# Kernel tuning notes

Measured on AMD Instinct MI355X. Metric: run time of the kernel, lower is better.

The kernel has to match this reference:

```python
import jax, jax.numpy as jnp
import numpy as np

NBITS = 4
DIM = 768
HEADS = 12
HEAD_DIM = DIM // HEADS
B, N = 8, 1024
SCALE = HEAD_DIM ** -0.5


def round_ste(x):
    # round_pass: straight-through round
    return x + jax.lax.stop_gradient(jnp.round(x) - x)


def grad_scale(x, g):
    # forward: x, backward: grad * g
    return x * g + jax.lax.stop_gradient(x * (1.0 - g))


def actq(x, alpha, zp, signed):
    # ActQ eval-mode forward: per-channel alpha/zero_point collapsed via .mean()
    if signed:
        Qn, Qp = -2 ** (NBITS - 1), 2 ** (NBITS - 1) - 1
    else:
        Qn, Qp = 0, 2 ** NBITS - 1
    a = jnp.mean(alpha)
    z = jnp.mean(round_ste(zp))
    xq = round_ste(jnp.clip(x / a + z, Qn, Qp))
    return (xq - z) * a


def linearq(x, w, b, alpha_w, act_alpha, act_zp):
    # LSQ weight quant (per-out-channel alpha with grad_scale) + input ActQ
    Qn, Qp = -2 ** (NBITS - 1), 2 ** (NBITS - 1) - 1
    g = 1.0 / np.sqrt(w.size * Qp)
    a = grad_scale(alpha_w, g)[:, None]  # [out,1]
    w_q = round_ste(jnp.clip(w / a, Qn, Qp)) * a
    xq = actq(x, act_alpha, act_zp, signed=True)
    y = jnp.einsum('...i,oi->...o', xq, w_q)
    return y if b is None else y + b


def layernorm(x, g, b, eps=1e-5):
    m = jnp.mean(x, axis=-1, keepdims=True)
    v = jnp.var(x, axis=-1, keepdims=True)  # biased, matches torch LayerNorm
    return (x - m) / jnp.sqrt(v + eps) * g + b


def setup_inputs() -> dict:
    key = jax.random.key(0)
    ks = jax.random.split(key, 20)
    u = lambda k, shape: jax.random.uniform(k, shape, jnp.float32, 0.01, 0.05)
    zp = lambda k, shape: jax.random.uniform(k, shape, jnp.float32, -0.3, 0.3)
    return {
        'x0': jax.random.normal(ks[0], (B, N, DIM), jnp.float32),
        'qkv_w': jax.random.normal(ks[1], (3 * DIM, DIM), jnp.float32) * 0.02,
        'qkv_alpha_w': u(ks[2], (3 * DIM,)),
        'qkv_act_alpha': u(ks[3], (DIM,)),
        'qkv_act_zp': zp(ks[4], (DIM,)),
        'norm_q_g': jnp.ones((HEAD_DIM,), jnp.float32),
        'norm_q_b': jnp.zeros((HEAD_DIM,), jnp.float32),
        'norm_k_g': jnp.ones((HEAD_DIM,), jnp.float32),
        'norm_k_b': jnp.zeros((HEAD_DIM,), jnp.float32),
        'q_alpha': u(ks[5], (HEADS,)), 'q_zp': zp(ks[6], (HEADS,)),
        'k_alpha': u(ks[7], (HEADS,)), 'k_zp': zp(ks[8], (HEADS,)),
        'v_alpha': u(ks[9], (HEADS,)), 'v_zp': zp(ks[10], (HEADS,)),
        'attn_alpha': u(ks[11], (HEADS,)), 'attn_zp': zp(ks[12], (HEADS,)),
        'proj_w': jax.random.normal(ks[13], (DIM, DIM), jnp.float32) * 0.02,
        'proj_b': jnp.zeros((DIM,), jnp.float32),
        'proj_alpha_w': u(ks[14], (DIM,)),
        'proj_act_alpha': u(ks[15], (DIM,)),
        'proj_act_zp': zp(ks[16], (DIM,)),
    }


def reference(x0, qkv_w, qkv_alpha_w, qkv_act_alpha, qkv_act_zp,
              norm_q_g, norm_q_b, norm_k_g, norm_k_b,
              q_alpha, q_zp, k_alpha, k_zp, v_alpha, v_zp,
              attn_alpha, attn_zp,
              proj_w, proj_b, proj_alpha_w, proj_act_alpha, proj_act_zp):
    b, n, c = x0.shape
    qkv = linearq(x0, qkv_w, None, qkv_alpha_w, qkv_act_alpha, qkv_act_zp)
    qkv = qkv.reshape(b, n, 3, HEADS, HEAD_DIM).transpose(2, 0, 3, 1, 4)  # [3,B,H,N,hd]
    q0, k0, v0 = qkv[0], qkv[1], qkv[2]
    q1 = layernorm(q0, norm_q_g, norm_q_b)
    k1 = layernorm(k0, norm_k_g, norm_k_b)
    q2 = actq(q1, q_alpha, q_zp, signed=True)
    k2 = actq(k1, k_alpha, k_zp, signed=True)
    v2 = actq(v0, v_alpha, v_zp, signed=True)
    attn = jax.nn.softmax(jnp.einsum('bhqd,bhkd->bhqk', q2, k2) * SCALE, axis=-1)
    attn = actq(attn, attn_alpha, attn_zp, signed=False)  # softmax output is unsigned
    x1 = jnp.einsum('bhqk,bhkd->bhqd', attn, v2).transpose(0, 2, 1, 3).reshape(b, n, c)
    return linearq(x1, proj_w, proj_b, proj_alpha_w, proj_act_alpha, proj_act_zp)
```

## Files before the change

kernel.cpp:

```cpp
#include <hip/hip_runtime.h>
#include <hip/hip_bf16.h>

#define HEADS 12
#define HD 64
#define DIM 768
#define SEQ 1024
#define NTOK 8192
#define TRIPLE 2304
#define BHTOT 96

typedef __attribute__((ext_vector_type(8))) short bf16x8;
typedef __attribute__((ext_vector_type(4))) float f32x4;

#define MFMA_B16(a, b, c) __builtin_amdgcn_mfma_f32_16x16x32_bf16((a), (b), (c), 0, 0, 0)

__device__ __forceinline__ unsigned short f2bf(float f) {
  unsigned int u = __float_as_uint(f);
  unsigned int r = (u + 0x7fffu + ((u >> 16) & 1u)) >> 16;
  return (unsigned short)r;
}
__device__ __forceinline__ float qclamp(float v, float lo, float hi) {
  return fminf(fmaxf(v, lo), hi);
}

__device__ float block_mean(const float* p, int n, int rnd, float* red) {
  int t = threadIdx.x;
  float s = 0.f;
  for (int i = t; i < n; i += 256) { float v = p[i]; s += rnd ? rintf(v) : v; }
  red[t] = s;
  __syncthreads();
  for (int o = 128; o > 0; o >>= 1) { if (t < o) red[t] += red[t + o]; __syncthreads(); }
  float m = red[0] / (float)n;
  __syncthreads();
  return m;
}

__global__ __launch_bounds__(256) void k_prep(
    const float* qaa, const float* qzp, const float* qa, const float* qz,
    const float* ka, const float* kz, const float* va, const float* vz,
    const float* ata, const float* atz, const float* pa, const float* pz,
    float* sc) {
  __shared__ float red[256];
  float r0 = block_mean(qaa, 768, 0, red);
  float r1 = block_mean(qzp, 768, 1, red);
  float r2 = block_mean(qa, 12, 0, red);
  float r3 = block_mean(qz, 12, 1, red);
  float r4 = block_mean(ka, 12, 0, red);
  float r5 = block_mean(kz, 12, 1, red);
  float r6 = block_mean(va, 12, 0, red);
  float r7 = block_mean(vz, 12, 1, red);
  float r8 = block_mean(ata, 12, 0, red);
  float r9 = block_mean(atz, 12, 1, red);
  float r10 = block_mean(pa, 768, 0, red);
  float r11 = block_mean(pz, 768, 1, red);
  if (threadIdx.x == 0) {
    sc[0] = r0; sc[1] = r1; sc[2] = r2; sc[3] = r3; sc[4] = r4; sc[5] = r5;
    sc[6] = r6; sc[7] = r7; sc[8] = r8; sc[9] = r9; sc[10] = r10; sc[11] = r11;
  }
}

__global__ __launch_bounds__(256) void k_quant_act(
    const float* __restrict__ x, unsigned short* __restrict__ xq,
    const float* __restrict__ sc, int n) {
  int i = (blockIdx.x * 256 + threadIdx.x) * 4;
  if (i >= n) return;
  float a = sc[0], z = sc[1];
  float4 v = *(const float4*)(x + i);
  ushort4 o;
  o.x = f2bf(rintf(qclamp(v.x / a + z, -8.f, 7.f)) - z);
  o.y = f2bf(rintf(qclamp(v.y / a + z, -8.f, 7.f)) - z);
  o.z = f2bf(rintf(qclamp(v.z / a + z, -8.f, 7.f)) - z);
  o.w = f2bf(rintf(qclamp(v.w / a + z, -8.f, 7.f)) - z);
  *(ushort4*)(xq + i) = o;
}

__global__ __launch_bounds__(256) void k_quant_w(
    const float* __restrict__ w, const float* __restrict__ alpha,
    unsigned short* __restrict__ wq, int n, int K) {
  int i = (blockIdx.x * 256 + threadIdx.x) * 4;
  if (i >= n) return;
  float a = alpha[i / K];
  float4 v = *(const float4*)(w + i);
  ushort4 o;
  o.x = f2bf(rintf(qclamp(v.x / a, -8.f, 7.f)));
  o.y = f2bf(rintf(qclamp(v.y / a, -8.f, 7.f)));
  o.z = f2bf(rintf(qclamp(v.z / a, -8.f, 7.f)));
  o.w = f2bf(rintf(qclamp(v.w / a, -8.f, 7.f)));
  *(ushort4*)(wq + i) = o;
}

__device__ __forceinline__ void stage128x64(
    const unsigned short* __restrict__ g, int ldk,
    unsigned short* lds, int wv, int l) {
#pragma unroll
  for (int j = 0; j < 4; ++j) {
    __builtin_amdgcn_global_load_lds(
        (const __attribute__((address_space(1))) void*)(
            g + (size_t)(wv * 32 + j * 8 + (l >> 3)) * ldk + (l & 7) * 8),
        (__attribute__((address_space(3))) void*)(lds + wv * 2048 + j * 512),
        16, 0, 0);
  }
}

__global__ __launch_bounds__(256) void k_gemm_qkv(
    const unsigned short* __restrict__ A, const unsigned short* __restrict__ Bw,
    const float* __restrict__ colscale, const float* __restrict__ sc,
    const float* __restrict__ nqg, const float* __restrict__ nqb,
    const float* __restrict__ nkg, const float* __restrict__ nkb,
    unsigned short* __restrict__ q2b, unsigned short* __restrict__ k2b,
    unsigned short* __restrict__ v2t) {
  __shared__ unsigned short As[128 * 64];
  __shared__ unsigned short Bs[128 * 64];
  const int t = threadIdx.x;
  const int brow = blockIdx.x * 128, bcol = blockIdx.y * 128;
  const int w = t >> 6, l = t & 63;
  const int lr = l & 15, lg = l >> 4;
  const int wr = (w >> 1) * 64, wc = (w & 1) * 64;
  f32x4 acc[4][4] = {};
  for (int kt = 0; kt < DIM; kt += 64) {
    __syncthreads();
    stage128x64(A + (size_t)brow * DIM + kt, DIM, As, w, l);
    stage128x64(Bw + (size_t)bcol * DIM + kt, DIM, Bs, w, l);
    __syncthreads();
#pragma unroll
    for (int ks = 0; ks < 2; ++ks) {
      bf16x8 af[4], bfr[4];
#pragma unroll
      for (int i = 0; i < 4; ++i) {
        af[i] = *(const bf16x8*)&As[(wr + i * 16 + lr) * 64 + ks * 32 + lg * 8];
        bfr[i] = *(const bf16x8*)&Bs[(wc + i * 16 + lr) * 64 + ks * 32 + lg * 8];
      }
#pragma unroll
      for (int i = 0; i < 4; ++i)
#pragma unroll
        for (int j = 0; j < 4; ++j)
          acc[i][j] = MFMA_B16(af[i], bfr[j], acc[i][j]);
    }
  }
  const float sact = sc[0];
  float s_j[4];
#pragma unroll
  for (int j = 0; j < 4; ++j) s_j[j] = sact * colscale[bcol + wc + j * 16 + lr];
#pragma unroll
  for (int i = 0; i < 4; ++i)
#pragma unroll
    for (int j = 0; j < 4; ++j)
#pragma unroll
      for (int r = 0; r < 4; ++r) acc[i][j][r] *= s_j[j];

  const int seg = bcol / DIM;
  const int h_ = ((bcol % DIM) + wc) / 64;
  if (seg < 2) {
    const float* gp = seg ? nkg : nqg;
    const float* bp = seg ? nkb : nqb;
    const float aq_ = seg ? sc[4] : sc[2];
    const float zq_ = seg ? sc[5] : sc[3];
    float gj[4], bj[4];
#pragma unroll
    for (int j = 0; j < 4; ++j) { gj[j] = gp[j * 16 + lr]; bj[j] = bp[j * 16 + lr]; }
    unsigned short* dstb = seg ? k2b : q2b;
#pragma unroll
    for (int i = 0; i < 4; ++i)
#pragma unroll
      for (int r = 0; r < 4; ++r) {
        float sum = acc[i][0][r] + acc[i][1][r] + acc[i][2][r] + acc[i][3][r];
        sum += __shfl_xor(sum, 1); sum += __shfl_xor(sum, 2);
        sum += __shfl_xor(sum, 4); sum += __shfl_xor(sum, 8);
        float m = sum * (1.0f / 64.0f);
        float vs = 0.f;
#pragma unroll
        for (int j = 0; j < 4; ++j) { float d = acc[i][j][r] - m; vs += d * d; }
        vs += __shfl_xor(vs, 1); vs += __shfl_xor(vs, 2);
        vs += __shfl_xor(vs, 4); vs += __shfl_xor(vs, 8);
        float inv = 1.0f / sqrtf(vs * (1.0f / 64.0f) + 1e-5f);
        int row = brow + wr + i * 16 + lg * 4 + r;
        int b_ = row >> 10, n_ = row & (SEQ - 1);
        unsigned short* dst = dstb + (((size_t)(b_ * HEADS + h_) << 10) + n_) * HD;
#pragma unroll
        for (int j = 0; j < 4; ++j) {
          float yv = (acc[i][j][r] - m) * inv * gj[j] + bj[j];
          float qv = rintf(qclamp(yv / aq_ + zq_, -8.f, 7.f)) - zq_;
          dst[j * 16 + lr] = f2bf(qv);
        }
      }
  } else {
    const float av_ = sc[6], zv = sc[7];
#pragma unroll
    for (int i = 0; i < 4; ++i)
#pragma unroll
      for (int r = 0; r < 4; ++r) {
        int row = brow + wr + i * 16 + lg * 4 + r;
        int b_ = row >> 10, n_ = row & (SEQ - 1);
        unsigned short* dst = v2t + ((size_t)(b_ * HEADS + h_) << 16) + n_;
#pragma unroll
        for (int j = 0; j < 4; ++j) {
          float qv = rintf(qclamp(acc[i][j][r] / av_ + zv, -8.f, 7.f)) - zv;
          dst[(size_t)(j * 16 + lr) * SEQ] = f2bf(qv);
        }
      }
  }
}

__global__ __launch_bounds__(256) void k_gemm(
    const unsigned short* __restrict__ A, const unsigned short* __restrict__ Bw,
    float* __restrict__ out, const float* __restrict__ colscale,
    const float* __restrict__ bias, const float* __restrict__ sc, int sact_idx,
    int M, int Nt, int K) {
  __shared__ unsigned short As[128 * 64];
  __shared__ unsigned short Bs[128 * 64];
  const int t = threadIdx.x;
  const int brow = blockIdx.x * 128, bcol = blockIdx.y * 128;
  const int w = t >> 6, l = t & 63;
  const int lr = l & 15, lg = l >> 4;
  const int wr = (w >> 1) * 64, wc = (w & 1) * 64;
  f32x4 acc[4][4] = {};
  for (int kt = 0; kt < K; kt += 64) {
    __syncthreads();
    stage128x64(A + (size_t)brow * K + kt, K, As, w, l);
    stage128x64(Bw + (size_t)bcol * K + kt, K, Bs, w, l);
    __syncthreads();
#pragma unroll
    for (int ks = 0; ks < 2; ++ks) {
      bf16x8 af[4], bfr[4];
#pragma unroll
      for (int i = 0; i < 4; ++i) {
        af[i] = *(const bf16x8*)&As[(wr + i * 16 + lr) * 64 + ks * 32 + lg * 8];
        bfr[i] = *(const bf16x8*)&Bs[(wc + i * 16 + lr) * 64 + ks * 32 + lg * 8];
      }
#pragma unroll
      for (int i = 0; i < 4; ++i)
#pragma unroll
        for (int j = 0; j < 4; ++j)
          acc[i][j] = MFMA_B16(af[i], bfr[j], acc[i][j]);
    }
  }
  const float sact = sc[sact_idx];
#pragma unroll
  for (int j = 0; j < 4; ++j) {
    const int col = bcol + wc + j * 16 + lr;
    const float s = sact * colscale[col];
    const float bb = bias ? bias[col] : 0.f;
#pragma unroll
    for (int i = 0; i < 4; ++i) {
      const int row0 = brow + wr + i * 16 + lg * 4;
#pragma unroll
      for (int r = 0; r < 4; ++r)
        out[(size_t)(row0 + r) * Nt + col] = acc[i][j][r] * s + bb;
    }
  }
}

__global__ __launch_bounds__(256, 3) void k_attn(
    const unsigned short* __restrict__ q2b, const unsigned short* __restrict__ k2b,
    const unsigned short* __restrict__ v2t, unsigned short* __restrict__ x1q,
    const float* __restrict__ sc) {
  __shared__ unsigned short Ks[128][72];
  __shared__ unsigned short Vs[64][136];
  __shared__ unsigned short Ps[4][32][40];
  const int t = threadIdx.x;
  const int w = t >> 6, l = t & 63;
  const int lr = l & 15, lg = l >> 4;
  const int bid = (int)(blockIdx.x & 7) * 96 + (int)(blockIdx.x >> 3);
  const int bh = bid >> 3, qc = bid & 7;
  const unsigned short* Qg = q2b + (size_t)bh * (SEQ * HD);
  const unsigned short* Kg = k2b + (size_t)bh * (SEQ * HD);
  const unsigned short* Vg = v2t + (size_t)bh * (SEQ * HD);
  const float aq = sc[2], ak = sc[4], av_ = sc[6], aa = sc[8], za = sc[9];
  const float ap = sc[10], zpp = sc[11];
  const float sqk2 = aq * ak * 0.125f * 1.44269504f;
  const float spv = aa * av_;
  const int qr0 = qc * 128 + w * 32;

  bf16x8 qf[2][2];
#pragma unroll
  for (int rt = 0; rt < 2; ++rt)
#pragma unroll
    for (int ks = 0; ks < 2; ++ks)
      qf[rt][ks] = *(const bf16x8*)(Qg + (size_t)(qr0 + rt * 16 + lr) * HD + ks * 32 + lg * 8);

  const int sr = t >> 1, sc0 = (t & 1) * 32;
  const int vr = t >> 2, vc0 = (t & 3) * 32;

  float lacc[2][4] = {};
  for (int kt = 0; kt < SEQ; kt += 128) {
    const uint4* g = (const uint4*)(Kg + (size_t)(kt + sr) * HD + sc0);
    uint4 u0 = g[0], u1 = g[1], u2 = g[2], u3 = g[3];
    __syncthreads();
    { uint4* d = (uint4*)&Ks[sr][sc0]; d[0] = u0; d[1] = u1; d[2] = u2; d[3] = u3; }
    __syncthreads();
#pragma unroll
    for (int ct = 0; ct < 8; ++ct) {
      const int kl = ct * 16 + lr;
      bf16x8 kf0 = *(const bf16x8*)&Ks[kl][lg * 8];
      bf16x8 kf1 = *(const bf16x8*)&Ks[kl][32 + lg * 8];
#pragma unroll
      for (int rt = 0; rt < 2; ++rt) {
        f32x4 s4 = {0.f, 0.f, 0.f, 0.f};
        s4 = MFMA_B16(qf[rt][0], kf0, s4);
        s4 = MFMA_B16(qf[rt][1], kf1, s4);
#pragma unroll
        for (int r = 0; r < 4; ++r)
          lacc[rt][r] += __builtin_amdgcn_exp2f(s4[r] * sqk2);
      }
    }
  }
#pragma unroll
  for (int off = 1; off < 16; off <<= 1)
#pragma unroll
    for (int rt = 0; rt < 2; ++rt)
#pragma unroll
      for (int r = 0; r < 4; ++r) lacc[rt][r] += __shfl_xor(lacc[rt][r], off);
  float pinv[2][4];
#pragma unroll
  for (int rt = 0; rt < 2; ++rt)
#pragma unroll
    for (int r = 0; r < 4; ++r) pinv[rt][r] = 1.0f / (lacc[rt][r] * aa);

  f32x4 oacc[2][4] = {};
  for (int kt = 0; kt < SEQ; kt += 128) {
    const uint4* gk = (const uint4*)(Kg + (size_t)(kt + sr) * HD + sc0);
    uint4 u0 = gk[0], u1 = gk[1], u2 = gk[2], u3 = gk[3];
    const uint4* gv = (const uint4*)(Vg + (size_t)vr * SEQ + kt + vc0);
    uint4 w0 = gv[0], w1 = gv[1], w2 = gv[2], w3 = gv[3];
    __syncthreads();
    { uint4* d = (uint4*)&Ks[sr][sc0]; d[0] = u0; d[1] = u1; d[2] = u2; d[3] = u3; }
    { uint4* d = (uint4*)&Vs[vr][vc0]; d[0] = w0; d[1] = w1; d[2] = w2; d[3] = w3; }
    __syncthreads();
#pragma unroll
    for (int q4 = 0; q4 < 4; ++q4) {
#pragma unroll
      for (int c2 = 0; c2 < 2; ++c2) {
        const int ct = q4 * 2 + c2;
        const int kl = ct * 16 + lr;
        bf16x8 kf0 = *(const bf16x8*)&Ks[kl][lg * 8];
        bf16x8 kf1 = *(const bf16x8*)&Ks[kl][32 + lg * 8];
#pragma unroll
        for (int rt = 0; rt < 2; ++rt) {
          f32x4 s4 = {0.f, 0.f, 0.f, 0.f};
          s4 = MFMA_B16(qf[rt][0], kf0, s4);
          s4 = MFMA_B16(qf[rt][1], kf1, s4);
#pragma unroll
          for (int r = 0; r < 4; ++r) {
            float e = __builtin_amdgcn_exp2f(s4[r] * sqk2);
            float p = fmaf(e, pinv[rt][r], za);
            float qv = rintf(qclamp(p, 0.f, 15.f)) - za;
            Ps[w][rt * 16 + lg * 4 + r][c2 * 16 + lr] = f2bf(qv);
          }
        }
      }
      bf16x8 vf[4], pf[2];
#pragma unroll
      for (int dt = 0; dt < 4; ++dt)
        vf[dt] = *(const bf16x8*)&Vs[dt * 16 + lr][q4 * 32 + lg * 8];
#pragma unroll
      for (int rt = 0; rt < 2; ++rt)
        pf[rt] = *(const bf16x8*)&Ps[w][rt * 16 + lr][lg * 8];
#pragma unroll
      for (int rt = 0; rt < 2; ++rt)
#pragma unroll
        for (int dt = 0; dt < 4; ++dt)
          oacc[rt][dt] = MFMA_B16(pf[rt], vf[dt], oacc[rt][dt]);
    }
  }
  const int b_ = bh / HEADS, h_ = bh % HEADS;
#pragma unroll
  for (int rt = 0; rt < 2; ++rt)
#pragma unroll
    for (int dt = 0; dt < 4; ++dt) {
      const int col = h_ * HD + dt * 16 + lr;
#pragma unroll
      for (int r = 0; r < 4; ++r) {
        const int qrow = qr0 + rt * 16 + lg * 4 + r;
        float x1v = oacc[rt][dt][r] * spv;
        float xv = rintf(qclamp(x1v / ap + zpp, -8.f, 7.f)) - zpp;
        x1q[(size_t)(b_ * SEQ + qrow) * DIM + col] = f2bf(xv);
      }
    }
}

extern "C" void kernel_launch(void* const* d_in, const int* in_sizes, int n_in,
                              void* d_out, int out_size, void* d_ws, size_t ws_size,
                              hipStream_t stream) {
  const float* x0      = (const float*)d_in[0];
  const float* qkvw    = (const float*)d_in[1];
  const float* qkv_aw  = (const float*)d_in[2];
  const float* qkv_aa  = (const float*)d_in[3];
  const float* qkv_azp = (const float*)d_in[4];
  const float* nqg     = (const float*)d_in[5];
  const float* nqb     = (const float*)d_in[6];
  const float* nkg     = (const float*)d_in[7];
  const float* nkb     = (const float*)d_in[8];
  const float* q_a     = (const float*)d_in[9];
  const float* q_z     = (const float*)d_in[10];
  const float* k_a     = (const float*)d_in[11];
  const float* k_z     = (const float*)d_in[12];
  const float* v_a     = (const float*)d_in[13];
  const float* v_z     = (const float*)d_in[14];
  const float* at_a    = (const float*)d_in[15];
  const float* at_z    = (const float*)d_in[16];
  const float* pw      = (const float*)d_in[17];
  const float* pb      = (const float*)d_in[18];
  const float* p_aw    = (const float*)d_in[19];
  const float* p_aa    = (const float*)d_in[20];
  const float* p_azp   = (const float*)d_in[21];
  float* out = (float*)d_out;

  char* ws = (char*)d_ws;
  size_t off = 0;
  float* scal = (float*)(ws); off = 256;
  unsigned short* x0q  = (unsigned short*)(ws + off); off += (size_t)NTOK * DIM * 2;
  unsigned short* qwq  = (unsigned short*)(ws + off); off += (size_t)TRIPLE * DIM * 2;
  unsigned short* pwq  = (unsigned short*)(ws + off); off += (size_t)DIM * DIM * 2;
  unsigned short* q2b  = (unsigned short*)(ws + off); off += (size_t)BHTOT * SEQ * HD * 2;
  unsigned short* k2b  = (unsigned short*)(ws + off); off += (size_t)BHTOT * SEQ * HD * 2;
  unsigned short* v2t  = (unsigned short*)(ws + off); off += (size_t)BHTOT * SEQ * HD * 2;
  unsigned short* x1q  = (unsigned short*)(ws + off); off += (size_t)NTOK * DIM * 2;

  k_prep<<<1, 256, 0, stream>>>(qkv_aa, qkv_azp, q_a, q_z, k_a, k_z, v_a, v_z,
                                at_a, at_z, p_aa, p_azp, scal);
  k_quant_act<<<(NTOK * DIM) / 1024, 256, 0, stream>>>(x0, x0q, scal, NTOK * DIM);
  k_quant_w<<<(TRIPLE * DIM) / 1024, 256, 0, stream>>>(qkvw, qkv_aw, qwq, TRIPLE * DIM, DIM);
  k_quant_w<<<(DIM * DIM) / 1024, 256, 0, stream>>>(pw, p_aw, pwq, DIM * DIM, DIM);
  k_gemm_qkv<<<dim3(NTOK / 128, TRIPLE / 128), 256, 0, stream>>>(
      x0q, qwq, qkv_aw, scal, nqg, nqb, nkg, nkb, q2b, k2b, v2t);
  k_attn<<<BHTOT * 8, 256, 0, stream>>>(q2b, k2b, v2t, x1q, scal);
  k_gemm<<<dim3(NTOK / 128, DIM / 128), 256, 0, stream>>>(
      x1q, pwq, out, p_aw, pb, scal, 10, NTOK, DIM, DIM);
}
```

Baseline: 291.1 us.

## Switch linear GEMMs to int8 MFMA with zero-point correction via weight row sums

Quantized activations and weights are now stored as int8 codes instead of bf16 values, and both linear GEMMs use the i32 16x16x64 int8 MFMA with K tiles of 128. Because the activation zero point is no longer folded into the stored values, a new kernel computes per-output-row weight sums so the epilogue can subtract zin*wsum before scaling. This halves the operand bytes and doubles the per-instruction K depth. The cost is an extra small kernel launch and exact integer-to-float conversions in the epilogue. The attention kernel now writes int8 codes for the projection input.

```diff
diff --git a/kernel.cpp b/kernel.cpp
--- a/kernel.cpp
+++ b/kernel.cpp
@@ -11,8 +11,10 @@
 
 typedef __attribute__((ext_vector_type(8))) short bf16x8;
 typedef __attribute__((ext_vector_type(4))) float f32x4;
+typedef __attribute__((ext_vector_type(4))) int i32x4;
 
 #define MFMA_B16(a, b, c) __builtin_amdgcn_mfma_f32_16x16x32_bf16((a), (b), (c), 0, 0, 0)
+#define MFMA_I8(a, b, c) __builtin_amdgcn_mfma_i32_16x16x64_i8((a), (b), (c), 0, 0, 0)
 
 __device__ __forceinline__ unsigned short f2bf(float f) {
   unsigned int u = __float_as_uint(f);
@@ -60,93 +62,114 @@
 }
 
 __global__ __launch_bounds__(256) void k_quant_act(
-    const float* __restrict__ x, unsigned short* __restrict__ xq,
+    const float* __restrict__ x, signed char* __restrict__ xq,
     const float* __restrict__ sc, int n) {
   int i = (blockIdx.x * 256 + threadIdx.x) * 4;
   if (i >= n) return;
   float a = sc[0], z = sc[1];
   float4 v = *(const float4*)(x + i);
-  ushort4 o;
-  o.x = f2bf(rintf(qclamp(v.x / a + z, -8.f, 7.f)) - z);
-  o.y = f2bf(rintf(qclamp(v.y / a + z, -8.f, 7.f)) - z);
-  o.z = f2bf(rintf(qclamp(v.z / a + z, -8.f, 7.f)) - z);
-  o.w = f2bf(rintf(qclamp(v.w / a + z, -8.f, 7.f)) - z);
-  *(ushort4*)(xq + i) = o;
+  int b0 = (int)rintf(qclamp(v.x / a + z, -8.f, 7.f));
+  int b1 = (int)rintf(qclamp(v.y / a + z, -8.f, 7.f));
+  int b2 = (int)rintf(qclamp(v.z / a + z, -8.f, 7.f));
+  int b3 = (int)rintf(qclamp(v.w / a + z, -8.f, 7.f));
+  ((int*)xq)[i >> 2] = (b0 & 255) | ((b1 & 255) << 8) | ((b2 & 255) << 16) | (b3 << 24);
 }
 
 __global__ __launch_bounds__(256) void k_quant_w(
     const float* __restrict__ w, const float* __restrict__ alpha,
-    unsigned short* __restrict__ wq, int n, int K) {
+    signed char* __restrict__ wq, int n, int K) {
   int i = (blockIdx.x * 256 + threadIdx.x) * 4;
   if (i >= n) return;
   float a = alpha[i / K];
   float4 v = *(const float4*)(w + i);
-  ushort4 o;
-  o.x = f2bf(rintf(qclamp(v.x / a, -8.f, 7.f)));
-  o.y = f2bf(rintf(qclamp(v.y / a, -8.f, 7.f)));
-  o.z = f2bf(rintf(qclamp(v.z / a, -8.f, 7.f)));
-  o.w = f2bf(rintf(qclamp(v.w / a, -8.f, 7.f)));
-  *(ushort4*)(wq + i) = o;
-}
-
-__device__ __forceinline__ void stage128x64(
-    const unsigned short* __restrict__ g, int ldk,
-    unsigned short* lds, int wv, int l) {
+  int b0 = (int)rintf(qclamp(v.x / a, -8.f, 7.f));
+  int b1 = (int)rintf(qclamp(v.y / a, -8.f, 7.f));
+  int b2 = (int)rintf(qclamp(v.z / a, -8.f, 7.f));
+  int b3 = (int)rintf(qclamp(v.w / a, -8.f, 7.f));
+  ((int*)wq)[i >> 2] = (b0 & 255) | ((b1 & 255) << 8) | ((b2 & 255) << 16) | (b3 << 24);
+}
+
+__global__ __launch_bounds__(256) void k_wsum(
+    const signed char* __restrict__ wq, float* __restrict__ s, int K) {
+  const int w = threadIdx.x >> 6, l = threadIdx.x & 63;
+  const int row = blockIdx.x * 4 + w;
+  const int* rp = (const int*)(wq + (size_t)row * K);
+  int acc = 0;
+  for (int idx = l; idx < K / 4; idx += 64) {
+    int u = rp[idx];
+    acc += (int)(signed char)u + (int)(signed char)(u >> 8) +
+           (int)(signed char)(u >> 16) + (int)(signed char)(u >> 24);
+  }
+#pragma unroll
+  for (int off = 32; off > 0; off >>= 1) acc += __shfl_xor(acc, off);
+  if (l == 0) s[row] = (float)acc;
+}
+
+__device__ __forceinline__ void stage_i8(
+    const signed char* __restrict__ g, int ldk,
+    signed char* lds, int wv, int l) {
 #pragma unroll
   for (int j = 0; j < 4; ++j) {
     __builtin_amdgcn_global_load_lds(
         (const __attribute__((address_space(1))) void*)(
-            g + (size_t)(wv * 32 + j * 8 + (l >> 3)) * ldk + (l & 7) * 8),
-        (__attribute__((address_space(3))) void*)(lds + wv * 2048 + j * 512),
+            g + (size_t)(wv * 32 + j * 8 + (l >> 3)) * ldk + (l & 7) * 16),
+        (__attribute__((address_space(3))) void*)(lds + wv * 4096 + j * 1024),
         16, 0, 0);
   }
 }
 
 __global__ __launch_bounds__(256) void k_gemm_qkv(
-    const unsigned short* __restrict__ A, const unsigned short* __restrict__ Bw,
-    const float* __restrict__ colscale, const float* __restrict__ sc,
+    const signed char* __restrict__ A, const signed char* __restrict__ Bw,
+    const float* __restrict__ colscale, const float* __restrict__ wsum,
+    const float* __restrict__ sc,
     const float* __restrict__ nqg, const float* __restrict__ nqb,
     const float* __restrict__ nkg, const float* __restrict__ nkb,
     unsigned short* __restrict__ q2b, unsigned short* __restrict__ k2b,
     unsigned short* __restrict__ v2t) {
-  __shared__ unsigned short As[128 * 64];
-  __shared__ unsigned short Bs[128 * 64];
+  __shared__ signed char As[128 * 128];
+  __shared__ signed char Bs[128 * 128];
   const int t = threadIdx.x;
   const int brow = blockIdx.x * 128, bcol = blockIdx.y * 128;
   const int w = t >> 6, l = t & 63;
   const int lr = l & 15, lg = l >> 4;
   const int wr = (w >> 1) * 64, wc = (w & 1) * 64;
-  f32x4 acc[4][4] = {};
-  for (int kt = 0; kt < DIM; kt += 64) {
-    __syncthreads();
-    stage128x64(A + (size_t)brow * DIM + kt, DIM, As, w, l);
-    stage128x64(Bw + (size_t)bcol * DIM + kt, DIM, Bs, w, l);
+  i32x4 acc[4][4] = {};
+  for (int kt = 0; kt < DIM; kt += 128) {
+    __syncthreads();
+    stage_i8(A + (size_t)brow * DIM + kt, DIM, As, w, l);
+    stage_i8(Bw + (size_t)bcol * DIM + kt, DIM, Bs, w, l);
     __syncthreads();
 #pragma unroll
     for (int ks = 0; ks < 2; ++ks) {
-      bf16x8 af[4], bfr[4];
+      i32x4 af[4], bfr[4];
 #pragma unroll
       for (int i = 0; i < 4; ++i) {
-        af[i] = *(const bf16x8*)&As[(wr + i * 16 + lr) * 64 + ks * 32 + lg * 8];
-        bfr[i] = *(const bf16x8*)&Bs[(wc + i * 16 + lr) * 64 + ks * 32 + lg * 8];
+        af[i] = *(const i32x4*)&As[(wr + i * 16 + lr) * 128 + ks * 64 + lg * 16];
+        bfr[i] = *(const i32x4*)&Bs[(wc + i * 16 + lr) * 128 + ks * 64 + lg * 16];
       }
 #pragma unroll
       for (int i = 0; i < 4; ++i)
 #pragma unroll
         for (int j = 0; j < 4; ++j)
-          acc[i][j] = MFMA_B16(af[i], bfr[j], acc[i][j]);
-    }
-  }
-  const float sact = sc[0];
-  float s_j[4];
-#pragma unroll
-  for (int j = 0; j < 4; ++j) s_j[j] = sact * colscale[bcol + wc + j * 16 + lr];
+          acc[i][j] = MFMA_I8(af[i], bfr[j], acc[i][j]);
+    }
+  }
+  const float sact = sc[0], zin = sc[1];
+  float s_j[4], zw_j[4];
+#pragma unroll
+  for (int j = 0; j < 4; ++j) {
+    const int col = bcol + wc + j * 16 + lr;
+    s_j[j] = sact * colscale[col];
+    zw_j[j] = zin * wsum[col];
+  }
+  f32x4 fac[4][4];
 #pragma unroll
   for (int i = 0; i < 4; ++i)
 #pragma unroll
     for (int j = 0; j < 4; ++j)
 #pragma unroll
-      for (int r = 0; r < 4; ++r) acc[i][j][r] *= s_j[j];
+      for (int r = 0; r < 4; ++r)
+        fac[i][j][r] = ((float)acc[i][j][r] - zw_j[j]) * s_j[j];
 
   const int seg = bcol / DIM;
   const int h_ = ((bcol % DIM) + wc) / 64;
@@ -163,13 +186,13 @@
     for (int i = 0; i < 4; ++i)
 #pragma unroll
       for (int r = 0; r < 4; ++r) {
-        float sum = acc[i][0][r] + acc[i][1][r] + acc[i][2][r] + acc[i][3][r];
+        float sum = fac[i][0][r] + fac[i][1][r] + fac[i][2][r] + fac[i][3][r];
         sum += __shfl_xor(sum, 1); sum += __shfl_xor(sum, 2);
         sum += __shfl_xor(sum, 4); sum += __shfl_xor(sum, 8);
         float m = sum * (1.0f / 64.0f);
         float vs = 0.f;
 #pragma unroll
-        for (int j = 0; j < 4; ++j) { float d = acc[i][j][r] - m; vs += d * d; }
+        for (int j = 0; j < 4; ++j) { float d = fac[i][j][r] - m; vs += d * d; }
         vs += __shfl_xor(vs, 1); vs += __shfl_xor(vs, 2);
         vs += __shfl_xor(vs, 4); vs += __shfl_xor(vs, 8);
         float inv = 1.0f / sqrtf(vs * (1.0f / 64.0f) + 1e-5f);
@@ -178,7 +201,7 @@
         unsigned short* dst = dstb + (((size_t)(b_ * HEADS + h_) << 10) + n_) * HD;
 #pragma unroll
         for (int j = 0; j < 4; ++j) {
-          float yv = (acc[i][j][r] - m) * inv * gj[j] + bj[j];
+          float yv = (fac[i][j][r] - m) * inv * gj[j] + bj[j];
           float qv = rintf(qclamp(yv / aq_ + zq_, -8.f, 7.f)) - zq_;
           dst[j * 16 + lr] = f2bf(qv);
         }
@@ -194,7 +217,7 @@
         unsigned short* dst = v2t + ((size_t)(b_ * HEADS + h_) << 16) + n_;
 #pragma unroll
         for (int j = 0; j < 4; ++j) {
-          float qv = rintf(qclamp(acc[i][j][r] / av_ + zv, -8.f, 7.f)) - zv;
+          float qv = rintf(qclamp(fac[i][j][r] / av_ + zv, -8.f, 7.f)) - zv;
           dst[(size_t)(j * 16 + lr) * SEQ] = f2bf(qv);
         }
       }
@@ -202,57 +225,59 @@
 }
 
 __global__ __launch_bounds__(256) void k_gemm(
-    const unsigned short* __restrict__ A, const unsigned short* __restrict__ Bw,
+    const signed char* __restrict__ A, const signed char* __restrict__ Bw,
     float* __restrict__ out, const float* __restrict__ colscale,
-    const float* __restrict__ bias, const float* __restrict__ sc, int sact_idx,
+    const float* __restrict__ wsum, const float* __restrict__ bias,
+    const float* __restrict__ sc, int sact_idx, int zin_idx,
     int M, int Nt, int K) {
-  __shared__ unsigned short As[128 * 64];
-  __shared__ unsigned short Bs[128 * 64];
+  __shared__ signed char As[128 * 128];
+  __shared__ signed char Bs[128 * 128];
   const int t = threadIdx.x;
   const int brow = blockIdx.x * 128, bcol = blockIdx.y * 128;
   const int w = t >> 6, l = t & 63;
   const int lr = l & 15, lg = l >> 4;
   const int wr = (w >> 1) * 64, wc = (w & 1) * 64;
-  f32x4 acc[4][4] = {};
-  for (int kt = 0; kt < K; kt += 64) {
-    __syncthreads();
-    stage128x64(A + (size_t)brow * K + kt, K, As, w, l);
-    stage128x64(Bw + (size_t)bcol * K + kt, K, Bs, w, l);
+  i32x4 acc[4][4] = {};
+  for (int kt = 0; kt < K; kt += 128) {
+    __syncthreads();
+    stage_i8(A + (size_t)brow * K + kt, K, As, w, l);
+    stage_i8(Bw + (size_t)bcol * K + kt, K, Bs, w, l);
     __syncthreads();
 #pragma unroll
     for (int ks = 0; ks < 2; ++ks) {
-      bf16x8 af[4], bfr[4];
+      i32x4 af[4], bfr[4];
 #pragma unroll
       for (int i = 0; i < 4; ++i) {
-        af[i] = *(const bf16x8*)&As[(wr + i * 16 + lr) * 64 + ks * 32 + lg * 8];
-        bfr[i] = *(const bf16x8*)&Bs[(wc + i * 16 + lr) * 64 + ks * 32 + lg * 8];
+        af[i] = *(const i32x4*)&As[(wr + i * 16 + lr) * 128 + ks * 64 + lg * 16];
+        bfr[i] = *(const i32x4*)&Bs[(wc + i * 16 + lr) * 128 + ks * 64 + lg * 16];
       }
 #pragma unroll
       for (int i = 0; i < 4; ++i)
 #pragma unroll
         for (int j = 0; j < 4; ++j)
-          acc[i][j] = MFMA_B16(af[i], bfr[j], acc[i][j]);
-    }
-  }
-  const float sact = sc[sact_idx];
+          acc[i][j] = MFMA_I8(af[i], bfr[j], acc[i][j]);
+    }
+  }
+  const float sact = sc[sact_idx], zin = sc[zin_idx];
 #pragma unroll
   for (int j = 0; j < 4; ++j) {
     const int col = bcol + wc + j * 16 + lr;
     const float s = sact * colscale[col];
+    const float zw = zin * wsum[col];
     const float bb = bias ? bias[col] : 0.f;
 #pragma unroll
     for (int i = 0; i < 4; ++i) {
       const int row0 = brow + wr + i * 16 + lg * 4;
 #pragma unroll
       for (int r = 0; r < 4; ++r)
-        out[(size_t)(row0 + r) * Nt + col] = acc[i][j][r] * s + bb;
+        out[(size_t)(row0 + r) * Nt + col] = ((float)acc[i][j][r] - zw) * s + bb;
     }
   }
 }
 
 __global__ __launch_bounds__(256, 3) void k_attn(
     const unsigned short* __restrict__ q2b, const unsigned short* __restrict__ k2b,
-    const unsigned short* __restrict__ v2t, unsigned short* __restrict__ x1q,
+    const unsigned short* __restrict__ v2t, signed char* __restrict__ x1q,
     const float* __restrict__ sc) {
   __shared__ unsigned short Ks[128][72];
   __shared__ unsigned short Vs[64][136];
@@ -372,8 +397,8 @@
       for (int r = 0; r < 4; ++r) {
         const int qrow = qr0 + rt * 16 + lg * 4 + r;
         float x1v = oacc[rt][dt][r] * spv;
-        float xv = rintf(qclamp(x1v / ap + zpp, -8.f, 7.f)) - zpp;
-        x1q[(size_t)(b_ * SEQ + qrow) * DIM + col] = f2bf(xv);
+        int xi = (int)rintf(qclamp(x1v / ap + zpp, -8.f, 7.f));
+        x1q[(size_t)(b_ * SEQ + qrow) * DIM + col] = (signed char)xi;
       }
     }
 }
@@ -408,22 +433,26 @@
   char* ws = (char*)d_ws;
   size_t off = 0;
   float* scal = (float*)(ws); off = 256;
-  unsigned short* x0q  = (unsigned short*)(ws + off); off += (size_t)NTOK * DIM * 2;
-  unsigned short* qwq  = (unsigned short*)(ws + off); off += (size_t)TRIPLE * DIM * 2;
-  unsigned short* pwq  = (unsigned short*)(ws + off); off += (size_t)DIM * DIM * 2;
-  unsigned short* q2b  = (unsigned short*)(ws + off); off += (size_t)BHTOT * SEQ * HD * 2;
-  unsigned short* k2b  = (unsigned short*)(ws + off); off += (size_t)BHTOT * SEQ * HD * 2;
-  unsigned short* v2t  = (unsigned short*)(ws + off); off += (size_t)BHTOT * SEQ * HD * 2;
-  unsigned short* x1q  = (unsigned short*)(ws + off); off += (size_t)NTOK * DIM * 2;
+  signed char* x0q  = (signed char*)(ws + off); off += (size_t)NTOK * DIM;
+  signed char* qwq  = (signed char*)(ws + off); off += (size_t)TRIPLE * DIM;
+  signed char* pwq  = (signed char*)(ws + off); off += (size_t)DIM * DIM;
+  float* wsumQ      = (float*)(ws + off);       off += (size_t)TRIPLE * 4;
+  float* wsumP      = (float*)(ws + off);       off += (size_t)DIM * 4;
+  unsigned short* q2b = (unsigned short*)(ws + off); off += (size_t)BHTOT * SEQ * HD * 2;
+  unsigned short* k2b = (unsigned short*)(ws + off); off += (size_t)BHTOT * SEQ * HD * 2;
+  unsigned short* v2t = (unsigned short*)(ws + off); off += (size_t)BHTOT * SEQ * HD * 2;
+  signed char* x1q  = (signed char*)(ws + off); off += (size_t)NTOK * DIM;
 
   k_prep<<<1, 256, 0, stream>>>(qkv_aa, qkv_azp, q_a, q_z, k_a, k_z, v_a, v_z,
                                 at_a, at_z, p_aa, p_azp, scal);
   k_quant_act<<<(NTOK * DIM) / 1024, 256, 0, stream>>>(x0, x0q, scal, NTOK * DIM);
   k_quant_w<<<(TRIPLE * DIM) / 1024, 256, 0, stream>>>(qkvw, qkv_aw, qwq, TRIPLE * DIM, DIM);
   k_quant_w<<<(DIM * DIM) / 1024, 256, 0, stream>>>(pw, p_aw, pwq, DIM * DIM, DIM);
+  k_wsum<<<TRIPLE / 4, 256, 0, stream>>>(qwq, wsumQ, DIM);
+  k_wsum<<<DIM / 4, 256, 0, stream>>>(pwq, wsumP, DIM);
   k_gemm_qkv<<<dim3(NTOK / 128, TRIPLE / 128), 256, 0, stream>>>(
-      x0q, qwq, qkv_aw, scal, nqg, nqb, nkg, nkb, q2b, k2b, v2t);
+      x0q, qwq, qkv_aw, wsumQ, scal, nqg, nqb, nkg, nkb, q2b, k2b, v2t);
   k_attn<<<BHTOT * 8, 256, 0, stream>>>(q2b, k2b, v2t, x1q, scal);
   k_gemm<<<dim3(NTOK / 128, DIM / 128), 256, 0, stream>>>(
-      x1q, pwq, out, p_aw, pb, scal, 10, NTOK, DIM, DIM);
-}
+      x1q, pwq, out, p_aw, wsumP, pb, scal, 10, 11, NTOK, DIM, DIM);
+}
```

New measurement: 270.5 us. -7.1%, faster.
